# Performance work log

Measured on AMD Instinct MI355X. Metric: run time of the kernel, lower is better.

The kernel has to match this reference:

```python
import jax, jax.numpy as jnp
import numpy as np
from jax import lax

DN = ('NCDHW', 'OIDHW', 'NCDHW')

def _reflect_conv(s, w, pad_dhw):
    # s: [B,2,D,H,W]; reflect-pad spatial dims then VALID conv -> same spatial size
    p = jnp.pad(s, ((0, 0), (0, 0)) + pad_dhw, mode='reflect')
    return lax.conv_general_dilated(p, w, window_strides=(1, 1, 1),
                                    padding='VALID', dimension_numbers=DN)

def setup_inputs() -> dict:
    key = jax.random.key(0)
    k = jax.random.split(key, 5)
    x = jax.random.normal(k[0], (4, 32, 16, 128, 128), dtype=jnp.float32)
    w1 = jax.random.normal(k[1], (1, 2, 7, 7, 5), dtype=jnp.float32) * 0.1
    w2 = jax.random.normal(k[2], (1, 2, 5, 5, 3), dtype=jnp.float32) * 0.1
    w3 = jax.random.normal(k[3], (1, 2, 3, 3, 1), dtype=jnp.float32) * 0.2
    wf = jax.random.normal(k[4], (1, 3, 1, 1, 1), dtype=jnp.float32) * 0.5
    return {'x': x, 'w1': w1, 'w2': w2, 'w3': w3, 'wf': wf}

def reference(x, w1, w2, w3, wf):
    # channel pool: mean & max over channel dim -> [B,2,D,H,W]
    s_in = jnp.concatenate([jnp.mean(x, axis=1, keepdims=True),
                            jnp.max(x, axis=1, keepdims=True)], axis=1)
    # branch pads in (D,H,W) order match kernels (7,7,5)/(5,5,3)/(3,3,1)
    s1 = _reflect_conv(s_in, w1, ((3, 3), (3, 3), (2, 2)))
    s2 = _reflect_conv(s_in, w2, ((2, 2), (2, 2), (1, 1)))
    s3 = _reflect_conv(s_in, w3, ((1, 1), (1, 1), (0, 0)))
    s = jnp.concatenate([s1, s2, s3], axis=1)  # [B,3,D,H,W]
    fused = lax.conv_general_dilated(s, wf, window_strides=(1, 1, 1),
                                     padding='VALID', dimension_numbers=DN)
    spatial_weight = jax.nn.sigmoid(fused)  # [B,1,D,H,W]
    return x * spatial_weight
```

## Files before the change

### kernel.cpp

```cpp
#include <hip/hip_runtime.h>
#include <math.h>

#define B_ 4
#define C_ 32
#define D_ 16
#define H_ 128
#define W_ 128
#define HW_ (H_*W_)
#define SP_ (D_*HW_)

typedef float f32x4 __attribute__((ext_vector_type(4)));
typedef float f32x4u __attribute__((ext_vector_type(4), aligned(4)));

__device__ __forceinline__ int refl(int i, int n) {
    i = (i < 0) ? -i : i;
    i = (i >= n) ? (2*n - 2 - i) : i;
    return i;
}

__global__ void prep_weights_kernel(const float* __restrict__ w1,
                                    const float* __restrict__ w2,
                                    const float* __restrict__ w3,
                                    const float* __restrict__ wf,
                                    float* __restrict__ Wc) {
    int t = blockIdx.x * blockDim.x + threadIdx.x;
    if (t >= 2*7*7*5) return;
    int ow = t % 5;
    int oh = (t / 5) % 7;
    int od = (t / 35) % 7;
    int ci = t / 245;
    float v = wf[0] * w1[((ci*7+od)*7+oh)*5+ow];
    if (od>=1 && od<=5 && oh>=1 && oh<=5 && ow>=1 && ow<=3)
        v = fmaf(wf[1], w2[((ci*5+(od-1))*5+(oh-1))*3+(ow-1)], v);
    if (od>=2 && od<=4 && oh>=2 && oh<=4 && ow==2)
        v = fmaf(wf[2], w3[(ci*3+(od-2))*3+(oh-2)], v);
    Wc[t] = v;
}

__global__ __launch_bounds__(256) void pool_kernel(const float* __restrict__ x,
                                                   float* __restrict__ s) {
    int t = blockIdx.x * blockDim.x + threadIdx.x;
    if (t >= B_*D_*H_*(W_/4)) return;
    int w4 = (t % (W_/4)) * 4;
    int rest = t / (W_/4);
    int h = rest % H_;
    int bd = rest / H_;
    int d = bd % D_;
    int b = bd / D_;
    const float* xp = x + (b*C_*D_ + d)*HW_ + h*W_ + w4;
    f32x4 v = *(const f32x4*)xp;
    f32x4 sm = v, mx = v;
    #pragma unroll 8
    for (int c = 1; c < C_; ++c) {
        f32x4 u = *(const f32x4*)(xp + c*SP_);
        sm += u;
        mx.x=fmaxf(mx.x,u.x); mx.y=fmaxf(mx.y,u.y); mx.z=fmaxf(mx.z,u.z); mx.w=fmaxf(mx.w,u.w);
    }
    sm *= (1.0f/32.0f);
    *(f32x4*)(s + ((b*2+0)*D_ + d)*HW_ + h*W_ + w4) = sm;
    *(f32x4*)(s + ((b*2+1)*D_ + d)*HW_ + h*W_ + w4) = mx;
}

__global__ __launch_bounds__(256, 2) void spatial_att_kernel(
        const float* __restrict__ x,
        const float* __restrict__ s,
        const float* __restrict__ Wc,
        float* __restrict__ out) {
    int bid = blockIdx.x;
    int ht = bid & 15;
    int dp = (bid >> 4) & 7;
    int b  = bid >> 7;
    int t = threadIdx.x;
    int w0 = (t & 31) * 4;
    int h0 = ht * 8 + (t >> 5);
    int d0 = dp * 2;

    const bool le = (t & 31) == 0;
    const bool re = (t & 31) == 31;
    const int offL = le ? 0 : -2;
    const int offR = re ? 0 :  2;

    int drow[8];
    #pragma unroll
    for (int k = 0; k < 8; ++k) drow[k] = refl(d0 + k - 3, D_) * HW_;

    float acc0[4] = {0.f, 0.f, 0.f, 0.f};
    float acc1[4] = {0.f, 0.f, 0.f, 0.f};

    for (int ci = 0; ci < 2; ++ci) {
        const float* sc = s + (b*2 + ci)*SP_;
        const float* wcb_ci = Wc + ci*245;
        for (int oh = 0; oh < 7; ++oh) {
            const float* sh = sc + refl(h0 + oh - 3, H_)*W_ + w0;
            const float* wcb = wcb_ci + oh*5;
            #pragma unroll
            for (int k = 0; k < 8; ++k) {
                const float* rp = sh + drow[k];
                const f32x4 L = *(const f32x4u*)(rp + offL);
                const f32x4 R = *(const f32x4u*)(rp + offR);
                float v[8];
                v[0] = le ? L.z : L.x;
                v[1] = L.y;
                v[2] = le ? L.x : L.z;
                v[3] = le ? L.y : L.w;
                v[4] = re ? R.z : R.x;
                v[5] = re ? R.w : R.y;
                v[6] = R.z;
                v[7] = re ? R.y : R.w;
                if (k <= 6) {
                    const float* wp = wcb + k*35;
                    #pragma unroll
                    for (int ow = 0; ow < 5; ++ow) {
                        float wgt = wp[ow];
                        #pragma unroll
                        for (int wi = 0; wi < 4; ++wi)
                            acc0[wi] = fmaf(wgt, v[wi+ow], acc0[wi]);
                    }
                }
                if (k >= 1) {
                    const float* wp = wcb + (k-1)*35;
                    #pragma unroll
                    for (int ow = 0; ow < 5; ++ow) {
                        float wgt = wp[ow];
                        #pragma unroll
                        for (int wi = 0; wi < 4; ++wi)
                            acc1[wi] = fmaf(wgt, v[wi+ow], acc1[wi]);
                    }
                }
            }
        }
    }

    float sg0[4], sg1[4];
    #pragma unroll
    for (int wi = 0; wi < 4; ++wi) {
        sg0[wi] = 1.0f/(1.0f + __expf(-acc0[wi]));
        sg1[wi] = 1.0f/(1.0f + __expf(-acc1[wi]));
    }

    int obase = (b*C_*D_ + d0)*HW_ + h0*W_ + w0;
    #pragma unroll 8
    for (int c = 0; c < C_; ++c) {
        int i0 = obase + c*SP_;
        f32x4 xv0 = *(const f32x4*)(x + i0);
        f32x4 xv1 = *(const f32x4*)(x + i0 + HW_);
        f32x4 o0; o0.x=xv0.x*sg0[0]; o0.y=xv0.y*sg0[1]; o0.z=xv0.z*sg0[2]; o0.w=xv0.w*sg0[3];
        f32x4 o1; o1.x=xv1.x*sg1[0]; o1.y=xv1.y*sg1[1]; o1.z=xv1.z*sg1[2]; o1.w=xv1.w*sg1[3];
        __builtin_nontemporal_store(o0, (f32x4*)(out + i0));
        __builtin_nontemporal_store(o1, (f32x4*)(out + i0 + HW_));
    }
}

extern "C" void kernel_launch(void* const* d_in, const int* in_sizes, int n_in,
                              void* d_out, int out_size, void* d_ws, size_t ws_size,
                              hipStream_t stream) {
    const float* x  = (const float*)d_in[0];
    const float* w1 = (const float*)d_in[1];
    const float* w2 = (const float*)d_in[2];
    const float* w3 = (const float*)d_in[3];
    const float* wf = (const float*)d_in[4];
    float* out = (float*)d_out;
    float* Wc = (float*)d_ws;
    float* s  = (float*)d_ws + 512;

    prep_weights_kernel<<<1, 512, 0, stream>>>(w1, w2, w3, wf, Wc);
    pool_kernel<<<(B_*D_*H_*(W_/4) + 255)/256, 256, 0, stream>>>(x, s);
    spatial_att_kernel<<<B_*(D_/2)*(H_/8), 256, 0, stream>>>(x, s, Wc, out);
}
```

Before: 86.04 us.

## Stage reflect-padded pooled planes in LDS with register prefetch of next plane

The conv stage now loads each reflect-padded 14x132 input plane slice cooperatively into shared memory. Each thread then reads its 7 rows of 8 values from LDS instead of issuing unaligned global loads per (oh,k) with edge-select logic. The next depth plane is prefetched into registers while the current one is consumed, giving software double buffering across the 16 plane iterations. This adds two block barriers per plane and extra LDS traffic in exchange for less redundant global/L2 traffic and simpler edge handling.

```diff
diff --git a/kernel.cpp b/kernel.cpp
--- a/kernel.cpp
+++ b/kernel.cpp
@@ -10,7 +10,6 @@
 #define SP_ (D_*HW_)
 
 typedef float f32x4 __attribute__((ext_vector_type(4)));
-typedef float f32x4u __attribute__((ext_vector_type(4), aligned(4)));
 
 __device__ __forceinline__ int refl(int i, int n) {
     i = (i < 0) ? -i : i;
@@ -66,49 +65,67 @@
         const float* __restrict__ s,
         const float* __restrict__ Wc,
         float* __restrict__ out) {
+    __shared__ float tile[14*132];
+
     int bid = blockIdx.x;
     int ht = bid & 15;
     int dp = (bid >> 4) & 7;
     int b  = bid >> 7;
     int t = threadIdx.x;
     int w0 = (t & 31) * 4;
-    int h0 = ht * 8 + (t >> 5);
+    int hh = t >> 5;
+    int h0b = ht * 8;
+    int h0 = h0b + hh;
     int d0 = dp * 2;
 
-    const bool le = (t & 31) == 0;
-    const bool re = (t & 31) == 31;
-    const int offL = le ? 0 : -2;
-    const int offR = re ? 0 :  2;
-
+    int gofs[8], lofs[8];
+    #pragma unroll
+    for (int i = 0; i < 8; ++i) {
+        int ei = t + 256*i; if (ei > 14*132-1) ei = 14*132-1;
+        int r = ei / 132, j = ei % 132;
+        gofs[i] = refl(h0b - 3 + r, H_) * W_ + refl(j - 2, W_);
+        lofs[i] = ei;
+    }
     int drow[8];
     #pragma unroll
     for (int k = 0; k < 8; ++k) drow[k] = refl(d0 + k - 3, D_) * HW_;
 
-    float acc0[4] = {0.f, 0.f, 0.f, 0.f};
-    float acc1[4] = {0.f, 0.f, 0.f, 0.f};
+    const float* sc0 = s + (b*2 + 0)*SP_;
+    const float* sc1 = s + (b*2 + 1)*SP_;
+
+    float acc0[4] = {0.f,0.f,0.f,0.f};
+    float acc1[4] = {0.f,0.f,0.f,0.f};
+
+    float g[8];
+    {
+        const float* sp0 = sc0 + drow[0];
+        #pragma unroll
+        for (int i = 0; i < 8; ++i) g[i] = sp0[gofs[i]];
+    }
 
     for (int ci = 0; ci < 2; ++ci) {
-        const float* sc = s + (b*2 + ci)*SP_;
+        const float* scc = ci ? sc1 : sc0;
         const float* wcb_ci = Wc + ci*245;
-        for (int oh = 0; oh < 7; ++oh) {
-            const float* sh = sc + refl(h0 + oh - 3, H_)*W_ + w0;
-            const float* wcb = wcb_ci + oh*5;
+        #pragma unroll
+        for (int k = 0; k < 8; ++k) {
+            __syncthreads();
             #pragma unroll
-            for (int k = 0; k < 8; ++k) {
-                const float* rp = sh + drow[k];
-                const f32x4 L = *(const f32x4u*)(rp + offL);
-                const f32x4 R = *(const f32x4u*)(rp + offR);
-                float v[8];
-                v[0] = le ? L.z : L.x;
-                v[1] = L.y;
-                v[2] = le ? L.x : L.z;
-                v[3] = le ? L.y : L.w;
-                v[4] = re ? R.z : R.x;
-                v[5] = re ? R.w : R.y;
-                v[6] = R.z;
-                v[7] = re ? R.y : R.w;
+            for (int i = 0; i < 8; ++i) tile[lofs[i]] = g[i];
+            if (!(ci == 1 && k == 7)) {
+                const int nk = (k + 1) & 7;
+                const float* np = ((k == 7) ? sc1 : scc) + drow[nk];
+                #pragma unroll
+                for (int i = 0; i < 8; ++i) g[i] = np[gofs[i]];
+            }
+            __syncthreads();
+            #pragma unroll
+            for (int oh = 0; oh < 7; ++oh) {
+                const float* lr = tile + (hh + oh)*132 + w0;
+                f32x4 A = *(const f32x4*)(lr);
+                f32x4 Bv = *(const f32x4*)(lr + 4);
+                float v[8] = {A.x, A.y, A.z, A.w, Bv.x, Bv.y, Bv.z, Bv.w};
                 if (k <= 6) {
-                    const float* wp = wcb + k*35;
+                    const float* wp = wcb_ci + k*35 + oh*5;
                     #pragma unroll
                     for (int ow = 0; ow < 5; ++ow) {
                         float wgt = wp[ow];
@@ -118,7 +135,7 @@
                     }
                 }
                 if (k >= 1) {
-                    const float* wp = wcb + (k-1)*35;
+                    const float* wp = wcb_ci + (k-1)*35 + oh*5;
                     #pragma unroll
                     for (int ow = 0; ow < 5; ++ow) {
                         float wgt = wp[ow];
```

Result: slower. 89.74 us (+4.3%).
